# Kernel tuning notes

Measured on AMD Instinct MI355X. Metric: run time of the kernel, lower is better.

The kernel has to match this reference:

```python
import jax, jax.numpy as jnp
from jax import lax
import numpy as np

PAD_IDX = 4
KERNEL_SIZES = (2, 3, 4, 5)
N_FILTERS = 32
D_EMB = 8
D_OUT = 64
VOCAB = 5
B, L = 4096, 512
LN_EPS = 1e-5


def setup_inputs() -> dict:
    key = jax.random.key(0)
    ks = jax.random.split(key, 32)
    inp = {}
    inp['x_idx'] = jax.random.randint(ks[0], (B, L), 0, VOCAB, dtype=jnp.int64 if jax.config.jax_enable_x64 else jnp.int32)
    emb = jax.random.normal(ks[1], (VOCAB, D_EMB), dtype=jnp.float32) * 0.1
    inp['emb'] = emb.at[PAD_IDX].set(0.0)  # padding_idx row zero
    for i, kz in enumerate(KERNEL_SIZES):
        inp[f'conv_w{i}'] = jax.random.normal(ks[2 + 2 * i], (N_FILTERS, D_EMB, kz), dtype=jnp.float32) * (1.0 / np.sqrt(D_EMB * kz))
        inp[f'conv_b{i}'] = jnp.zeros((N_FILTERS,), jnp.float32)
        inp[f'att_w{i}'] = jax.random.normal(ks[3 + 2 * i], (N_FILTERS,), dtype=jnp.float32) * (1.0 / np.sqrt(N_FILTERS))
        inp[f'att_b{i}'] = jnp.zeros((1,), jnp.float32)
    inp['proj_w'] = jax.random.normal(ks[20], (D_OUT, N_FILTERS * len(KERNEL_SIZES)), dtype=jnp.float32) * (1.0 / np.sqrt(N_FILTERS * len(KERNEL_SIZES)))
    inp['proj_b'] = jnp.zeros((D_OUT,), jnp.float32)
    inp['gamma'] = jnp.ones((D_OUT,), jnp.float32)
    inp['beta'] = jnp.zeros((D_OUT,), jnp.float32)
    return inp


def _branch(X, W, b, aw, ab):
    # X: [B, C_in, L]; W: [C_out, C_in, ks]
    h = lax.conv_general_dilated(X, W, (1,), 'VALID',
                                 dimension_numbers=('NCH', 'OIH', 'NCH'))
    h = jax.nn.gelu(h + b[None, :, None], approximate=False)     # [B, F, L']
    scores = jnp.einsum('bfl,f->bl', h, aw) + ab[0]              # linear attn score
    w = jax.nn.softmax(scores, axis=1)                           # over positions
    return jnp.einsum('bfl,bl->bf', h, w)                        # weighted pool -> [B, F]


def reference(x_idx, emb, conv_w0, conv_b0, conv_w1, conv_b1, conv_w2, conv_b2,
              conv_w3, conv_b3, att_w0, att_b0, att_w1, att_b1, att_w2, att_b2,
              att_w3, att_b3, proj_w, proj_b, gamma, beta):
    emb = emb.at[PAD_IDX].set(0.0)
    X = emb[x_idx].transpose(0, 2, 1)  # [B, d_emb, L]
    feats = [
        _branch(X, conv_w0, conv_b0, att_w0, att_b0),
        _branch(X, conv_w1, conv_b1, att_w1, att_b1),
        _branch(X, conv_w2, conv_b2, att_w2, att_b2),
        _branch(X, conv_w3, conv_b3, att_w3, att_b3),
    ]
    z = jnp.concatenate(feats, axis=1)                 # [B, 4*F]
    z = z @ proj_w.T + proj_b                          # [B, D_OUT]
    z = jax.nn.gelu(z, approximate=False)
    mu = jnp.mean(z, axis=-1, keepdims=True)
    var = jnp.var(z, axis=-1, keepdims=True)
    return (z - mu) / jnp.sqrt(var + LN_EPS) * gamma + beta
```

## Files before the change

kernel.cpp:

```cpp
#include <hip/hip_runtime.h>
#include <math.h>

typedef _Float16 half_t;
typedef _Float16 half8 __attribute__((ext_vector_type(8)));
typedef unsigned short ushort_t;

#define BATCH 4096
#define SEQL  512
#define NF    32
#define DEMB  8
#define DOUT  64

#define NWIN_TOTAL 3900
#define ZROW       3900
#define HWIN_OFF   4096
#define TOFF       70000
#define EHE_OFF    131072
#define MSHIFT     8.0f

__device__ __forceinline__ float gelu_exact(float x) {
    return 0.5f * x * (1.0f + erff(x * 0.70710678118654752f));
}

__global__ __launch_bounds__(256) void precompute_taps(
    const float* __restrict__ emb,
    const float* __restrict__ cw0, const float* __restrict__ cw1,
    const float* __restrict__ cw2, const float* __restrict__ cw3,
    float* __restrict__ ws)
{
    const int gid = blockIdx.x * blockDim.x + threadIdx.x;
    if (gid >= 14 * 5 * NF) return;
    const int f = gid & 31;
    const int r = gid >> 5;
    const int tapg = r / 5;
    const int d    = r % 5;

    int ks, t; const float* cw;
    if (tapg < 2)      { ks = 2; cw = cw0; t = tapg; }
    else if (tapg < 5) { ks = 3; cw = cw1; t = tapg - 2; }
    else if (tapg < 9) { ks = 4; cw = cw2; t = tapg - 5; }
    else               { ks = 5; cw = cw3; t = tapg - 9; }

    const float* e = emb + d * DEMB;
    float s = 0.0f;
#pragma unroll
    for (int c = 0; c < DEMB; ++c)
        s += e[c] * cw[(f * DEMB + c) * ks + t];
    ws[TOFF + r * NF + f] = s;
}

__global__ __launch_bounds__(256) void precompute_windows(
    const float* __restrict__ cb0, const float* __restrict__ aw0, const float* __restrict__ ab0,
    const float* __restrict__ cb1, const float* __restrict__ aw1, const float* __restrict__ ab1,
    const float* __restrict__ cb2, const float* __restrict__ aw2, const float* __restrict__ ab2,
    const float* __restrict__ cb3, const float* __restrict__ aw3, const float* __restrict__ ab3,
    float* __restrict__ ws)
{
    const int gid = blockIdx.x * blockDim.x + threadIdx.x;
    if (gid >= NWIN_TOTAL * NF) return;
    const int wgid = gid >> 5;
    const int f    = gid & 31;

    int w, ks, cum;
    const float *cb, *aw, *ab;
    if (wgid < 25)       { w = wgid;       ks = 2; cum = 0; cb = cb0; aw = aw0; ab = ab0; }
    else if (wgid < 150) { w = wgid - 25;  ks = 3; cum = 2; cb = cb1; aw = aw1; ab = ab1; }
    else if (wgid < 775) { w = wgid - 150; ks = 4; cum = 5; cb = cb2; aw = aw2; ab = ab2; }
    else                 { w = wgid - 775; ks = 5; cum = 9; cb = cb3; aw = aw3; ab = ab3; }

    float h = cb[f];
    int ww = w;
    for (int t = ks - 1; t >= 0; --t) {
        int d = ww % 5; ww /= 5;
        h += ws[TOFF + ((cum + t) * 5 + d) * NF + f];
    }
    float g = gelu_exact(h);
    ((half_t*)(ws + HWIN_OFF))[wgid * NF + f] = (half_t)g;

    float s = g * aw[f];
#pragma unroll
    for (int off = 16; off; off >>= 1) s += __shfl_xor(s, off, 32);
    if (f == 0) ws[wgid] = s + ab[0];
}

__global__ __launch_bounds__(256) void finalize_ehe(float* __restrict__ ws)
{
    const int gid = blockIdx.x * blockDim.x + threadIdx.x;
    if (gid >= (NWIN_TOTAL + 1) * 8) return;
    const int row = gid >> 3;
    const int seg = gid & 7;

    float4 v = {0.f, 0.f, 0.f, 0.f};
    if (row < NWIN_TOTAL) {
        const float E = __expf(ws[row] - MSHIFT);
        if (seg < 4) {
            const half_t* h = (const half_t*)(ws + HWIN_OFF) + row * NF + seg * 8;
            half_t o[8];
#pragma unroll
            for (int j = 0; j < 8; ++j) o[j] = (half_t)(E * (float)h[j]);
            v = *(const float4*)o;
        } else if (seg == 4) {
            v.x = E;
        }
    }
    *(float4*)((char*)(ws + EHE_OFF) + row * 128 + seg * 16) = v;
}

__global__ __launch_bounds__(256) void fused_main(
    const int*   __restrict__ xidx,
    const float* __restrict__ ws,
    const float* __restrict__ projw, const float* __restrict__ projb,
    const float* __restrict__ gamma, const float* __restrict__ beta,
    float* __restrict__ out)
{
    __shared__ int      xs[SEQL];
    __shared__ ushort_t pwid[4][SEQL];
    __shared__ float    feat[4 * NF];

    const int b   = blockIdx.x;
    const int tid = threadIdx.x;

#pragma unroll
    for (int i = tid; i < SEQL / 4; i += 256)
        ((int4*)xs)[i] = ((const int4*)(xidx + b * SEQL))[i];
    __syncthreads();

    const int wave = tid >> 6;
    const int lane = tid & 63;

    constexpr int KS[4]  = {2, 3, 4, 5};
    constexpr int SWB[4] = {0, 25, 150, 775};

    const int ks = KS[wave];
    const int Lp = SEQL + 1 - ks;

#pragma unroll
    for (int it = 0; it < 8; ++it) {
        const int l = lane + it * 64;
        ushort_t v = ZROW;
        if (l < Lp) {
            int w = xs[l];
            for (int t = 1; t < ks; ++t) w = w * 5 + xs[l + t];
            v = (ushort_t)(SWB[wave] + w);
        }
        pwid[wave][l] = v;
    }
    __syncthreads();

    const int r = lane & 7;
    const int o = lane >> 3;
    const int seg = (r < 4) ? r : 4;
    const char* base = (const char*)(ws + EHE_OFF) + seg * 16;

    float a[8];
#pragma unroll
    for (int j = 0; j < 8; ++j) a[j] = 0.0f;
    float den = 0.0f;

#pragma unroll 8
    for (int it = 0; it < 64; ++it) {
        const int pos = it * 8 + o;
        const int gid = pwid[wave][pos];
        const float4 rv = *(const float4*)(base + gid * 128);
        if (r < 4) {
            const half8 hv = *(const half8*)&rv;
#pragma unroll
            for (int j = 0; j < 8; ++j) a[j] += (float)hv[j];
        } else if (r == 4) {
            den += rv.x;
        }
    }

#pragma unroll
    for (int off = 8; off < 64; off <<= 1) {
#pragma unroll
        for (int j = 0; j < 8; ++j) a[j] += __shfl_xor(a[j], off);
        den += __shfl_xor(den, off);
    }
    const float dtot = __shfl(den, 4);
    if (lane < 4) {
        const float inv = 1.0f / dtot;
        float* fp = feat + wave * NF + lane * 8;
#pragma unroll
        for (int j = 0; j < 8; ++j) fp[j] = a[j] * inv;
    }
    __syncthreads();

    if (tid < DOUT) {
        float z = projb[tid];
        const float4* pwr = (const float4*)(projw + tid * (4 * NF));
#pragma unroll
        for (int q = 0; q < 32; ++q) {
            float4 wq = pwr[q];
            const float* fj = feat + q * 4;
            z += wq.x * fj[0] + wq.y * fj[1] + wq.z * fj[2] + wq.w * fj[3];
        }
        z = gelu_exact(z);

        float s1 = z, s2 = z * z;
#pragma unroll
        for (int off = 32; off; off >>= 1) {
            s1 += __shfl_xor(s1, off);
            s2 += __shfl_xor(s2, off);
        }
        const float mu  = s1 * (1.0f / 64.0f);
        const float var = s2 * (1.0f / 64.0f) - mu * mu;
        const float rr  = rsqrtf(var + 1e-5f);
        out[b * DOUT + tid] = (z - mu) * rr * gamma[tid] + beta[tid];
    }
}

extern "C" void kernel_launch(void* const* d_in, const int* in_sizes, int n_in,
                              void* d_out, int out_size, void* d_ws, size_t ws_size,
                              hipStream_t stream) {
    const int*   xidx = (const int*)d_in[0];
    const float* emb  = (const float*)d_in[1];
    const float* cw[4]; const float* cb[4]; const float* aw[4]; const float* ab[4];
    for (int i = 0; i < 4; ++i) {
        cw[i] = (const float*)d_in[2 + 4 * i];
        cb[i] = (const float*)d_in[3 + 4 * i];
        aw[i] = (const float*)d_in[4 + 4 * i];
        ab[i] = (const float*)d_in[5 + 4 * i];
    }
    const float* projw = (const float*)d_in[18];
    const float* projb = (const float*)d_in[19];
    const float* gm    = (const float*)d_in[20];
    const float* bt    = (const float*)d_in[21];
    float* ws  = (float*)d_ws;
    float* out = (float*)d_out;

    hipLaunchKernelGGL(precompute_taps, dim3((14 * 5 * NF + 255) / 256), dim3(256), 0, stream,
                       emb, cw[0], cw[1], cw[2], cw[3], ws);

    hipLaunchKernelGGL(precompute_windows, dim3((NWIN_TOTAL * NF + 255) / 256), dim3(256), 0, stream,
                       cb[0], aw[0], ab[0],
                       cb[1], aw[1], ab[1],
                       cb[2], aw[2], ab[2],
                       cb[3], aw[3], ab[3],
                       ws);

    hipLaunchKernelGGL(finalize_ehe, dim3(((NWIN_TOTAL + 1) * 8 + 255) / 256), dim3(256), 0, stream,
                       ws);

    hipLaunchKernelGGL(fused_main, dim3(BATCH), dim3(256), 0, stream,
                       xidx, ws, projw, projb, gm, bt, out);
}
```

Measured before the change: 163.2 us.

## Index all four branches by the 5-gram window via a combined table

Builds a combined 3125-row table keyed by the 5-token window, each 256-byte row holding the exp-weighted GELU features for all four kernel sizes. One gather per position now serves all branches, and positions are split across waves instead of branches. Softmax denominators come from a separate small fp16 exp table summed during window indexing, so the denominator lane in each row is no longer needed. This cuts the gather count and the shared-index traffic, but needs an extra cross-wave reduction through shared memory and a larger table with a less cache-friendly footprint.

```diff
diff --git a/kernel.cpp b/kernel.cpp
--- a/kernel.cpp
+++ b/kernel.cpp
@@ -12,8 +12,8 @@
 #define DOUT  64
 
 #define NWIN_TOTAL 3900
-#define ZROW       3900
 #define HWIN_OFF   4096
+#define ETAB_OFF   67000
 #define TOFF       70000
 #define EHE_OFF    131072
 #define MSHIFT     8.0f
@@ -80,30 +80,32 @@
     float s = g * aw[f];
 #pragma unroll
     for (int off = 16; off; off >>= 1) s += __shfl_xor(s, off, 32);
-    if (f == 0) ws[wgid] = s + ab[0];
-}
-
-__global__ __launch_bounds__(256) void finalize_ehe(float* __restrict__ ws)
+    if (f == 0)
+        ((half_t*)(ws + ETAB_OFF))[wgid] = (half_t)__expf(s + ab[0] - MSHIFT);
+}
+
+__global__ __launch_bounds__(256) void build_combined(float* __restrict__ ws)
 {
     const int gid = blockIdx.x * blockDim.x + threadIdx.x;
-    if (gid >= (NWIN_TOTAL + 1) * 8) return;
-    const int row = gid >> 3;
-    const int seg = gid & 7;
-
-    float4 v = {0.f, 0.f, 0.f, 0.f};
-    if (row < NWIN_TOTAL) {
-        const float E = __expf(ws[row] - MSHIFT);
-        if (seg < 4) {
-            const half_t* h = (const half_t*)(ws + HWIN_OFF) + row * NF + seg * 8;
-            half_t o[8];
-#pragma unroll
-            for (int j = 0; j < 8; ++j) o[j] = (half_t)(E * (float)h[j]);
-            v = *(const float4*)o;
-        } else if (seg == 4) {
-            v.x = E;
-        }
-    }
-    *(float4*)((char*)(ws + EHE_OFF) + row * 128 + seg * 16) = v;
+    if (gid >= 3125 * 16) return;
+    const int w5  = gid >> 4;
+    const int seg = gid & 15;
+    const int c   = seg >> 2;
+    const int q   = seg & 3;
+
+    int wc, swb;
+    if (c == 0)      { wc = w5 / 125; swb = 0;   }
+    else if (c == 1) { wc = w5 / 25;  swb = 25;  }
+    else if (c == 2) { wc = w5 / 5;   swb = 150; }
+    else             { wc = w5;       swb = 775; }
+    const int gw = swb + wc;
+
+    const float E = (float)((const half_t*)(ws + ETAB_OFF))[gw];
+    const half_t* hp = (const half_t*)(ws + HWIN_OFF) + gw * NF + q * 8;
+    half_t o[8];
+#pragma unroll
+    for (int j = 0; j < 8; ++j) o[j] = (half_t)(E * (float)hp[j]);
+    *(float4*)((char*)(ws + EHE_OFF) + w5 * 256 + seg * 16) = *(const float4*)o;
 }
 
 __global__ __launch_bounds__(256) void fused_main(
@@ -113,8 +115,10 @@
     const float* __restrict__ gamma, const float* __restrict__ beta,
     float* __restrict__ out)
 {
-    __shared__ int      xs[SEQL];
-    __shared__ ushort_t pwid[4][SEQL];
+    __shared__ int      xs[SEQL + 8];
+    __shared__ ushort_t pwid[SEQL];
+    __shared__ float    partial[4][16][8];
+    __shared__ float    redD[4][4];
     __shared__ float    feat[4 * NF];
 
     const int b   = blockIdx.x;
@@ -123,66 +127,78 @@
 #pragma unroll
     for (int i = tid; i < SEQL / 4; i += 256)
         ((int4*)xs)[i] = ((const int4*)(xidx + b * SEQL))[i];
+    if (tid < 8) xs[SEQL + tid] = 0;
     __syncthreads();
 
     const int wave = tid >> 6;
     const int lane = tid & 63;
-
-    constexpr int KS[4]  = {2, 3, 4, 5};
-    constexpr int SWB[4] = {0, 25, 150, 775};
-
-    const int ks = KS[wave];
-    const int Lp = SEQL + 1 - ks;
-
-#pragma unroll
-    for (int it = 0; it < 8; ++it) {
-        const int l = lane + it * 64;
-        ushort_t v = ZROW;
-        if (l < Lp) {
-            int w = xs[l];
-            for (int t = 1; t < ks; ++t) w = w * 5 + xs[l + t];
-            v = (ushort_t)(SWB[wave] + w);
+    const half_t* Etab = (const half_t*)(ws + ETAB_OFF);
+
+    float den0 = 0.f, den1 = 0.f, den2 = 0.f, den3 = 0.f;
+#pragma unroll
+    for (int it = 0; it < 2; ++it) {
+        const int l = wave * 128 + it * 64 + lane;
+        const int w2 = xs[l] * 5 + xs[l + 1];
+        const int w3 = w2 * 5 + xs[l + 2];
+        const int w4 = w3 * 5 + xs[l + 3];
+        const int w5 = w4 * 5 + xs[l + 4];
+        pwid[l] = (ushort_t)w5;
+        if (l < 511) den0 += (float)Etab[w2];
+        if (l < 510) den1 += (float)Etab[25 + w3];
+        if (l < 509) den2 += (float)Etab[150 + w4];
+        if (l < 508) den3 += (float)Etab[775 + w5];
+    }
+#pragma unroll
+    for (int off = 32; off; off >>= 1) {
+        den0 += __shfl_xor(den0, off);
+        den1 += __shfl_xor(den1, off);
+        den2 += __shfl_xor(den2, off);
+        den3 += __shfl_xor(den3, off);
+    }
+    if (lane == 0) {
+        redD[wave][0] = den0; redD[wave][1] = den1;
+        redD[wave][2] = den2; redD[wave][3] = den3;
+    }
+    __syncthreads();
+
+    const int seg = lane & 15;
+    const int o   = lane >> 4;
+    const int c   = seg >> 2;
+    const int Lpc = 511 - c;
+    const char* base = (const char*)(ws + EHE_OFF) + seg * 16;
+
+    float a[8];
+#pragma unroll
+    for (int j = 0; j < 8; ++j) a[j] = 0.0f;
+
+#pragma unroll 8
+    for (int it = 0; it < 32; ++it) {
+        const int pos = wave * 128 + it * 4 + o;
+        const int w5 = pwid[pos];
+        if (pos < Lpc) {
+            const float4 rv = *(const float4*)(base + w5 * 256);
+            const half8 hv = *(const half8*)&rv;
+#pragma unroll
+            for (int j = 0; j < 8; ++j) a[j] += (float)hv[j];
         }
-        pwid[wave][l] = v;
-    }
-    __syncthreads();
-
-    const int r = lane & 7;
-    const int o = lane >> 3;
-    const int seg = (r < 4) ? r : 4;
-    const char* base = (const char*)(ws + EHE_OFF) + seg * 16;
-
-    float a[8];
-#pragma unroll
-    for (int j = 0; j < 8; ++j) a[j] = 0.0f;
-    float den = 0.0f;
-
-#pragma unroll 8
-    for (int it = 0; it < 64; ++it) {
-        const int pos = it * 8 + o;
-        const int gid = pwid[wave][pos];
-        const float4 rv = *(const float4*)(base + gid * 128);
-        if (r < 4) {
-            const half8 hv = *(const half8*)&rv;
-#pragma unroll
-            for (int j = 0; j < 8; ++j) a[j] += (float)hv[j];
-        } else if (r == 4) {
-            den += rv.x;
-        }
-    }
-
-#pragma unroll
-    for (int off = 8; off < 64; off <<= 1) {
-#pragma unroll
-        for (int j = 0; j < 8; ++j) a[j] += __shfl_xor(a[j], off);
-        den += __shfl_xor(den, off);
-    }
-    const float dtot = __shfl(den, 4);
-    if (lane < 4) {
-        const float inv = 1.0f / dtot;
-        float* fp = feat + wave * NF + lane * 8;
-#pragma unroll
-        for (int j = 0; j < 8; ++j) fp[j] = a[j] * inv;
+    }
+
+#pragma unroll
+    for (int j = 0; j < 8; ++j) {
+        a[j] += __shfl_xor(a[j], 16);
+        a[j] += __shfl_xor(a[j], 32);
+    }
+    if (lane < 16) {
+#pragma unroll
+        for (int j = 0; j < 8; ++j) partial[wave][lane][j] = a[j];
+    }
+    __syncthreads();
+
+    if (tid < 128) {
+        const int sg = tid >> 3, j = tid & 7, cc = tid >> 5;
+        const float d = redD[0][cc] + redD[1][cc] + redD[2][cc] + redD[3][cc];
+        feat[tid] = (partial[0][sg][j] + partial[1][sg][j]
+                   + partial[2][sg][j] + partial[3][sg][j]) / d;
     }
     __syncthreads();
 
@@ -239,7 +255,7 @@
                        cb[3], aw[3], ab[3],
                        ws);
 
-    hipLaunchKernelGGL(finalize_ehe, dim3(((NWIN_TOTAL + 1) * 8 + 255) / 256), dim3(256), 0, stream,
+    hipLaunchKernelGGL(build_combined, dim3((3125 * 16 + 255) / 256), dim3(256), 0, stream,
                        ws);
 
     hipLaunchKernelGGL(fused_main, dim3(BATCH), dim3(256), 0, stream,
```

New measurement: 146.4 us. -10.3%, faster.
